# Optimization experiments

Hardware: AMD Instinct MI355X
Metric: run time of the kernel (lower is better)

## Reference

```python
import jax, jax.numpy as jnp
import numpy as np

RADIUS = 0.3      # extents/2, extents = radius_scale*6*particle_radius = 4*6*0.025 = 0.6
KSIZE = 4         # kernel_size [4,4,4]
KMAX = 80         # padded neighbor count
N = 50000
BOX = 5.2         # box side -> ~40 neighbors within RADIUS on average
CIN = 3
COUT = 3
_PI = 3.14159265358979323846


def _build_neighbors(pos, radius, kmax):
    # fixed-radius search (L2), ignore_query_point=True, padded to kmax per row
    n = pos.shape[0]
    r2 = radius * radius
    sq = (pos * pos).sum(1)
    idx = np.zeros((n, kmax), np.int32)
    msk = np.zeros((n, kmax), np.bool_)
    ch = 2500
    for s in range(0, n, ch):
        e = min(s + ch, n)
        d2 = sq[s:e, None] + sq[None, :] - 2.0 * (pos[s:e] @ pos.T)
        d2[np.arange(e - s), np.arange(s, e)] = np.inf  # radius_search_ignore_query_points
        rows, cols = np.nonzero(d2 < r2)
        starts = np.searchsorted(rows, np.arange(e - s))
        slot = np.arange(len(rows)) - starts[rows]
        keep = slot < kmax
        idx[rows[keep] + s, slot[keep]] = cols[keep]
        msk[rows[keep] + s, slot[keep]] = True
    return idx, msk


def setup_inputs():
    key = jax.random.key(0)
    k1, k2, k3 = jax.random.split(key, 3)
    pos = jax.random.uniform(k1, (N, 3), jnp.float32) * BOX
    vel = jax.random.normal(k2, (N, 3), jnp.float32)
    # keras 'uniform' initializer: U(-0.05, 0.05)
    kernel = jax.random.uniform(k3, (KSIZE, KSIZE, KSIZE, CIN, COUT), jnp.float32, -0.05, 0.05)
    nidx, nmask = _build_neighbors(np.asarray(pos), RADIUS, KMAX)
    return {"pos": pos, "vel": vel, "kernel": kernel,
            "neighbor_idx": jnp.asarray(nidx), "neighbor_mask": jnp.asarray(nmask)}


def _ball_to_cube_volume_preserving(u):
    # Open3D CoordinateTransformation.h: MapSphereToCylinder then MapCylinderToCube
    eps = 1e-12
    x, y, z = u[..., 0], u[..., 1], u[..., 2]
    sq = x * x + y * y + z * z
    norm = jnp.sqrt(jnp.maximum(sq, eps))
    sq_xy = x * x + y * y
    # sphere -> cylinder
    top = (1.25 * z * z) > sq_xy
    s_top = jnp.sqrt(3.0 * norm / (norm + jnp.abs(z)))
    s_side = norm / jnp.sqrt(jnp.maximum(sq_xy, eps))
    x1 = jnp.where(top, x * s_top, x * s_side)
    y1 = jnp.where(top, y * s_top, y * s_side)
    z1 = jnp.where(top, jnp.sign(z) * norm, 1.5 * z)
    small = sq < eps
    x1 = jnp.where(small, x, x1)
    y1 = jnp.where(small, y, y1)
    z1 = jnp.where(small, z, z1)
    # cylinder -> cube (equal-area disc->square on xy)
    sq_xy1 = x1 * x1 + y1 * y1
    norm_xy = jnp.sqrt(jnp.maximum(sq_xy1, eps))
    xbig = jnp.abs(y1) <= jnp.abs(x1)
    sx = jnp.sign(x1) * norm_xy
    sy = jnp.sign(y1) * norm_xy
    safe_x = jnp.where(jnp.abs(x1) > eps, x1, 1.0)
    safe_y = jnp.where(jnp.abs(y1) > eps, y1, 1.0)
    x2 = jnp.where(xbig, sx, sy * (4.0 / _PI) * jnp.arctan(x1 / safe_y))
    y2 = jnp.where(xbig, sx * (4.0 / _PI) * jnp.arctan(y1 / safe_x), sy)
    small_xy = sq_xy1 < eps
    x2 = jnp.where(small_xy, x1, x2)
    y2 = jnp.where(small_xy, y1, y2)
    return x2, y2, z1


def _grid_coords(c):
    # align_corners=True: [-1,1] -> [0, KSIZE-1]; 'linear' interpolation clamps to border
    t = jnp.clip((c + 1.0) * (0.5 * (KSIZE - 1)), 0.0, KSIZE - 1.0)
    t0 = jnp.floor(t)
    i0 = t0.astype(jnp.int32)
    i1 = jnp.minimum(i0 + 1, KSIZE - 1)
    f = t - t0
    return (i0, i1), (1.0 - f, f)


def _cconv(pos, vel, kernel, neighbor_idx, neighbor_mask):
    n = pos.shape[0]
    rel = pos[neighbor_idx] - pos[:, None, :]              # [N,K,3]
    d2 = jnp.sum(rel * rel, -1)
    # window_poly6 on squared distance normalized by radius^2
    imp = jnp.clip((1.0 - d2 / (RADIUS * RADIUS)) ** 3, 0.0, 1.0)
    imp = imp * neighbor_mask.astype(vel.dtype)
    cx, cy, cz = _ball_to_cube_volume_preserving(rel / RADIUS)
    (xi0, xi1), (wx0, wx1) = _grid_coords(cx)
    (yi0, yi1), (wy0, wy1) = _grid_coords(cy)
    (zi0, zi1), (wz0, wz1) = _grid_coords(cz)
    phi = vel[neighbor_idx] * imp[..., None]               # [N,K,Cin]
    rows = jnp.arange(n)[:, None]
    # accumulate window*trilinear-weighted features into the 64 filter taps,
    # then contract once with the flattened kernel (math identical to per-pair
    # interp(W) @ feat since everything is linear)
    A = jnp.zeros((n, KSIZE * KSIZE * KSIZE, vel.shape[1]), vel.dtype)
    for zi, wz in ((zi0, wz0), (zi1, wz1)):
        for yi, wy in ((yi0, wy0), (yi1, wy1)):
            for xi, wx in ((xi0, wx0), (xi1, wx1)):
                corner = (zi * KSIZE + yi) * KSIZE + xi
                A = A.at[rows, corner].add((wz * wy * wx)[..., None] * phi)
    Wflat = kernel.reshape(KSIZE * KSIZE * KSIZE, kernel.shape[3], kernel.shape[4])
    return jnp.einsum('ngi,gio->no', A, Wflat)        # [N, COUT]


def reference(pos, vel, kernel, neighbor_idx, neighbor_mask):
    return _cconv(pos, vel, kernel, neighbor_idx, neighbor_mask)
```

## Files before the change

### kernel.cpp

```cpp
#include <hip/hip_runtime.h>
#include <math.h>

#define N_PART 50000
#define KMAX 80
#define KS 4
#define LPP 16

typedef __attribute__((ext_vector_type(8))) _Float16 h8;
typedef __attribute__((ext_vector_type(2))) _Float16 h2;

__device__ __forceinline__ float atan_poly(float t) {
    float t2 = t * t;
    float p = -0.01172120f;
    p = p * t2 + 0.05265332f;
    p = p * t2 - 0.11643287f;
    p = p * t2 + 0.19354346f;
    p = p * t2 - 0.33262347f;
    p = p * t2 + 0.99997726f;
    return t * p;
}

template <typename MT>
__device__ __forceinline__ int prefix_count(const MT* __restrict__ nmask, int base, int sub) {
    int lc = 0; bool more = true;
    #pragma unroll
    for (int i = 0; i < 5; ++i) {
        bool t = nmask[base + sub * 5 + i] != 0;
        lc += (more && t) ? 1 : 0;
        more = more && t;
    }
    bool full = (lc == 5);
    unsigned long long nb = __ballot(!full);
    int wl  = threadIdx.x & 63;
    int grp = wl >> 4;
    unsigned int gb = (unsigned int)((nb >> (16 * grp)) & 0xFFFFull);
    if (gb == 0) return KMAX;
    int fi  = __ffs(gb) - 1;
    int flc = __shfl(lc, (grp << 4) + fi, 64);
    return fi * 5 + flc;
}

struct PV { float px, py, pz, ux, uy, uz; };

__device__ __forceinline__ void load_pv(const float* __restrict__ pos,
                                        const float* __restrict__ vel,
                                        int i, PV& v) {
    v.px = pos[3*i];  v.py = pos[3*i+1];  v.pz = pos[3*i+2];
    v.ux = vel[3*i];  v.uy = vel[3*i+1];  v.uz = vel[3*i+2];
}

__device__ __forceinline__ void pair_contrib(
    const PV& n, float cpx, float cpy, float cpz,
    const _Float16* __restrict__ WsH, const float* __restrict__ Ws8,
    float& acc0, float& acc1, float& acc2)
{
    const float inv_r = 1.0f / 0.3f;
    const float eps   = 1e-12f;
    const float FOUR_OVER_PI = 1.27323954473516268615f;

    float rx = (n.px - cpx) * inv_r;
    float ry = (n.py - cpy) * inv_r;
    float rz = (n.pz - cpz) * inv_r;

    float sq = rx * rx + ry * ry + rz * rz;

    float t1  = 1.0f - sq;
    float imp = fmaxf(t1 * t1 * t1, 0.0f);

    float norm   = sqrtf(fmaxf(sq, eps));
    float sq_xy  = rx * rx + ry * ry;
    bool  top    = (1.25f * rz * rz) > sq_xy;
    float rsq_xy = __builtin_amdgcn_rsqf(fmaxf(sq_xy, eps));
    float s_top  = sqrtf(3.0f * norm * __builtin_amdgcn_rcpf(norm + fabsf(rz)));
    float s_side = norm * rsq_xy;
    float s  = top ? s_top : s_side;
    float z1 = top ? copysignf(norm, rz) : 1.5f * rz;

    float nxy = top ? (sq_xy * rsq_xy * s_top) : norm;
    bool  xb  = fabsf(ry) <= fabsf(rx);
    float num = xb ? ry : rx;
    float den = xb ? rx : ry;
    float sden = (fabsf(den) > eps) ? den : 1.0f;
    float t    = num * __builtin_amdgcn_rcpf(sden);
    float at   = atan_poly(t);
    float sd   = copysignf(nxy, den);
    float u    = sd * FOUR_OVER_PI * at;
    float x2   = xb ? sd : u;
    float y2   = xb ? u  : sd;

    float tx = fminf(fmaxf((x2 + 1.0f) * 1.5f, 0.0f), 3.0f);
    float ty = fminf(fmaxf((y2 + 1.0f) * 1.5f, 0.0f), 3.0f);
    float tz = fminf(fmaxf((z1 + 1.0f) * 1.5f, 0.0f), 3.0f);
    float fx0 = floorf(tx), fy0 = floorf(ty), fz0 = floorf(tz);
    int xi0 = (int)fx0, yi0 = (int)fy0, zi0 = (int)fz0;
    int xi1 = min(xi0 + 1, KS - 1);
    int yi1 = min(yi0 + 1, KS - 1);
    int zi1 = min(zi0 + 1, KS - 1);
    float wx1 = tx - fx0, wx0 = 1.0f - wx1;
    float wy1 = ty - fy0, wy0 = 1.0f - wy1;
    float wz1 = tz - fz0, wz0 = 1.0f - wz1;

    int   zia[2] = { zi0 << 4, zi1 << 4 };  float wza[2] = { wz0, wz1 };
    int   yia[2] = { yi0 << 2, yi1 << 2 };  float wya[2] = { wy0, wy1 };
    int   xia[2] = { xi0, xi1 };            float wxa[2] = { wx0, wx1 };

    h2 M01 = (h2)(_Float16)0.0f;
    h2 M23 = (h2)(_Float16)0.0f;
    h2 M45 = (h2)(_Float16)0.0f;
    h2 M67 = (h2)(_Float16)0.0f;
    float m8 = 0.0f;

    #pragma unroll
    for (int cz = 0; cz < 2; ++cz) {
        #pragma unroll
        for (int cy = 0; cy < 2; ++cy) {
            float wzy = wza[cz] * wya[cy];
            int   czy = zia[cz] + yia[cy];
            #pragma unroll
            for (int cx = 0; cx < 2; ++cx) {
                int corner = czy + xia[cx];
                h8 wv = *(const h8*)&WsH[corner << 3];
                float wf = wzy * wxa[cx];
                _Float16 wh = (_Float16)wf;
                h2 ww = { wh, wh };
                M01 += ww * __builtin_shufflevector(wv, wv, 0, 1);
                M23 += ww * __builtin_shufflevector(wv, wv, 2, 3);
                M45 += ww * __builtin_shufflevector(wv, wv, 4, 5);
                M67 += ww * __builtin_shufflevector(wv, wv, 6, 7);
                m8  += wf * Ws8[corner];
            }
        }
    }

    float m0 = (float)M01[0], m1 = (float)M01[1];
    float m2 = (float)M23[0], m3 = (float)M23[1];
    float m4 = (float)M45[0], m5 = (float)M45[1];
    float m6 = (float)M67[0], m7 = (float)M67[1];
    float s0 = n.ux * m0 + n.uy * m3 + n.uz * m6;
    float s1 = n.ux * m1 + n.uy * m4 + n.uz * m7;
    float s2 = n.ux * m2 + n.uy * m5 + n.uz * m8;
    acc0 += imp * s0;
    acc1 += imp * s1;
    acc2 += imp * s2;
}

__global__ __launch_bounds__(256) void cconv_kernel(
    const float* __restrict__ pos,
    const float* __restrict__ vel,
    const float* __restrict__ Wg,
    const int* __restrict__ nidx,
    const void* __restrict__ nmask,
    float* __restrict__ out)
{
    __shared__ _Float16 WsH[64 * 8];
    __shared__ float    Ws8[64];
    for (int t = threadIdx.x; t < 64 * 8; t += blockDim.x) {
        int g = t >> 3, r = t & 7;
        WsH[t] = (_Float16)Wg[g * 9 + r];
    }
    for (int t = threadIdx.x; t < 64; t += blockDim.x)
        Ws8[t] = Wg[t * 9 + 8];
    __syncthreads();

    int gid = blockIdx.x * blockDim.x + threadIdx.x;
    int p   = gid >> 4;
    int sub = gid & 15;
    if (p >= N_PART) return;

    const int base = p * KMAX;

    int idxs[5];
    #pragma unroll
    for (int m = 0; m < 5; ++m)
        idxs[m] = nidx[base + sub + (m << 4)];

    bool byteMask;
    {
        const unsigned* mw = (const unsigned*)nmask;
        int lane = threadIdx.x & 63;
        bool big = false;
        #pragma unroll
        for (int i = 0; i < 8; ++i)
            big |= (mw[lane + 64 * i] > 1u);
        byteMask = (__ballot(big) != 0ULL);
    }

    float cpx = pos[3 * p], cpy = pos[3 * p + 1], cpz = pos[3 * p + 2];

    int cnt;
    if (byteMask) cnt = prefix_count<unsigned char>((const unsigned char*)nmask, base, sub);
    else          cnt = prefix_count<int>((const int*)nmask, base, sub);

    PV A, An;
    load_pv(pos, vel, idxs[0], A);

    float acc0 = 0.0f, acc1 = 0.0f, acc2 = 0.0f;

    int m = 0;
    for (int k = sub; k < cnt; k += LPP) {
        int mn = min(m + 1, 4);
        load_pv(pos, vel, idxs[mn], An);

        pair_contrib(A, cpx, cpy, cpz, WsH, Ws8, acc0, acc1, acc2);

        A = An; ++m;
    }

    acc0 += __shfl_xor(acc0, 1); acc0 += __shfl_xor(acc0, 2);
    acc0 += __shfl_xor(acc0, 4); acc0 += __shfl_xor(acc0, 8);
    acc1 += __shfl_xor(acc1, 1); acc1 += __shfl_xor(acc1, 2);
    acc1 += __shfl_xor(acc1, 4); acc1 += __shfl_xor(acc1, 8);
    acc2 += __shfl_xor(acc2, 1); acc2 += __shfl_xor(acc2, 2);
    acc2 += __shfl_xor(acc2, 4); acc2 += __shfl_xor(acc2, 8);

    if (sub == 0) {
        out[p * 3 + 0] = acc0;
        out[p * 3 + 1] = acc1;
        out[p * 3 + 2] = acc2;
    }
}

extern "C" void kernel_launch(void* const* d_in, const int* in_sizes, int n_in,
                              void* d_out, int out_size, void* d_ws, size_t ws_size,
                              hipStream_t stream) {
    const float* pos   = (const float*)d_in[0];
    const float* vel   = (const float*)d_in[1];
    const float* Wg    = (const float*)d_in[2];
    const int*   nidx  = (const int*)d_in[3];
    const void*  nmask = d_in[4];
    float*       out   = (float*)d_out;

    int threads = 256;
    long long total = (long long)N_PART * LPP;
    int grid = (int)((total + threads - 1) / threads);
    cconv_kernel<<<grid, threads, 0, stream>>>(pos, vel, Wg, nidx, nmask, out);
}
```

Measured before the change: 29.16 us.

## Pad weights to 16 halves, use fract for weights, simplify neighbor count

Packs the 9 per-tap weights into a padded 16-half shared row so the ninth channel is accumulated in packed fp16 instead of a separate fp32 load and FMA. Replaces floor/subtract with int truncation plus fractf and folds the grid offset into an FMA. Replaces the ballot/ffs prefix-count with a strided mask popcount reduced by xor shuffles, and drops the dead s_side computation. The new count assumes masks are contiguous prefixes, accumulates the ninth channel at lower precision, and removing the p>=N_PART guard relies on the grid dividing exactly.

```diff
diff --git a/kernel.cpp b/kernel.cpp
--- a/kernel.cpp
+++ b/kernel.cpp
@@ -20,26 +20,6 @@
     return t * p;
 }
 
-template <typename MT>
-__device__ __forceinline__ int prefix_count(const MT* __restrict__ nmask, int base, int sub) {
-    int lc = 0; bool more = true;
-    #pragma unroll
-    for (int i = 0; i < 5; ++i) {
-        bool t = nmask[base + sub * 5 + i] != 0;
-        lc += (more && t) ? 1 : 0;
-        more = more && t;
-    }
-    bool full = (lc == 5);
-    unsigned long long nb = __ballot(!full);
-    int wl  = threadIdx.x & 63;
-    int grp = wl >> 4;
-    unsigned int gb = (unsigned int)((nb >> (16 * grp)) & 0xFFFFull);
-    if (gb == 0) return KMAX;
-    int fi  = __ffs(gb) - 1;
-    int flc = __shfl(lc, (grp << 4) + fi, 64);
-    return fi * 5 + flc;
-}
-
 struct PV { float px, py, pz, ux, uy, uz; };
 
 __device__ __forceinline__ void load_pv(const float* __restrict__ pos,
@@ -51,7 +31,7 @@
 
 __device__ __forceinline__ void pair_contrib(
     const PV& n, float cpx, float cpy, float cpz,
-    const _Float16* __restrict__ WsH, const float* __restrict__ Ws8,
+    const _Float16* __restrict__ WsHP,
     float& acc0, float& acc1, float& acc2)
 {
     const float inv_r = 1.0f / 0.3f;
@@ -72,8 +52,6 @@
     bool  top    = (1.25f * rz * rz) > sq_xy;
     float rsq_xy = __builtin_amdgcn_rsqf(fmaxf(sq_xy, eps));
     float s_top  = sqrtf(3.0f * norm * __builtin_amdgcn_rcpf(norm + fabsf(rz)));
-    float s_side = norm * rsq_xy;
-    float s  = top ? s_top : s_side;
     float z1 = top ? copysignf(norm, rz) : 1.5f * rz;
 
     float nxy = top ? (sq_xy * rsq_xy * s_top) : norm;
@@ -88,17 +66,17 @@
     float x2   = xb ? sd : u;
     float y2   = xb ? u  : sd;
 
-    float tx = fminf(fmaxf((x2 + 1.0f) * 1.5f, 0.0f), 3.0f);
-    float ty = fminf(fmaxf((y2 + 1.0f) * 1.5f, 0.0f), 3.0f);
-    float tz = fminf(fmaxf((z1 + 1.0f) * 1.5f, 0.0f), 3.0f);
-    float fx0 = floorf(tx), fy0 = floorf(ty), fz0 = floorf(tz);
-    int xi0 = (int)fx0, yi0 = (int)fy0, zi0 = (int)fz0;
+    float tx = fminf(fmaxf(x2 * 1.5f + 1.5f, 0.0f), 3.0f);
+    float ty = fminf(fmaxf(y2 * 1.5f + 1.5f, 0.0f), 3.0f);
+    float tz = fminf(fmaxf(z1 * 1.5f + 1.5f, 0.0f), 3.0f);
+    int xi0 = (int)tx, yi0 = (int)ty, zi0 = (int)tz;
+    float wx1 = __builtin_amdgcn_fractf(tx);
+    float wy1 = __builtin_amdgcn_fractf(ty);
+    float wz1 = __builtin_amdgcn_fractf(tz);
     int xi1 = min(xi0 + 1, KS - 1);
     int yi1 = min(yi0 + 1, KS - 1);
     int zi1 = min(zi0 + 1, KS - 1);
-    float wx1 = tx - fx0, wx0 = 1.0f - wx1;
-    float wy1 = ty - fy0, wy0 = 1.0f - wy1;
-    float wz1 = tz - fz0, wz0 = 1.0f - wz1;
+    float wx0 = 1.0f - wx1, wy0 = 1.0f - wy1, wz0 = 1.0f - wz1;
 
     int   zia[2] = { zi0 << 4, zi1 << 4 };  float wza[2] = { wz0, wz1 };
     int   yia[2] = { yi0 << 2, yi1 << 2 };  float wya[2] = { wy0, wy1 };
@@ -108,7 +86,7 @@
     h2 M23 = (h2)(_Float16)0.0f;
     h2 M45 = (h2)(_Float16)0.0f;
     h2 M67 = (h2)(_Float16)0.0f;
-    float m8 = 0.0f;
+    h2 M89 = (h2)(_Float16)0.0f;
 
     #pragma unroll
     for (int cz = 0; cz < 2; ++cz) {
@@ -119,15 +97,17 @@
             #pragma unroll
             for (int cx = 0; cx < 2; ++cx) {
                 int corner = czy + xia[cx];
-                h8 wv = *(const h8*)&WsH[corner << 3];
+                const _Float16* Wc = &WsHP[corner << 4];
+                h8 lo = *(const h8*)Wc;
+                h2 hi = *(const h2*)(Wc + 8);
                 float wf = wzy * wxa[cx];
                 _Float16 wh = (_Float16)wf;
                 h2 ww = { wh, wh };
-                M01 += ww * __builtin_shufflevector(wv, wv, 0, 1);
-                M23 += ww * __builtin_shufflevector(wv, wv, 2, 3);
-                M45 += ww * __builtin_shufflevector(wv, wv, 4, 5);
-                M67 += ww * __builtin_shufflevector(wv, wv, 6, 7);
-                m8  += wf * Ws8[corner];
+                M01 += ww * __builtin_shufflevector(lo, lo, 0, 1);
+                M23 += ww * __builtin_shufflevector(lo, lo, 2, 3);
+                M45 += ww * __builtin_shufflevector(lo, lo, 4, 5);
+                M67 += ww * __builtin_shufflevector(lo, lo, 6, 7);
+                M89 += ww * hi;
             }
         }
     }
@@ -136,6 +116,7 @@
     float m2 = (float)M23[0], m3 = (float)M23[1];
     float m4 = (float)M45[0], m5 = (float)M45[1];
     float m6 = (float)M67[0], m7 = (float)M67[1];
+    float m8 = (float)M89[0];
     float s0 = n.ux * m0 + n.uy * m3 + n.uz * m6;
     float s1 = n.ux * m1 + n.uy * m4 + n.uz * m7;
     float s2 = n.ux * m2 + n.uy * m5 + n.uz * m8;
@@ -152,20 +133,16 @@
     const void* __restrict__ nmask,
     float* __restrict__ out)
 {
-    __shared__ _Float16 WsH[64 * 8];
-    __shared__ float    Ws8[64];
-    for (int t = threadIdx.x; t < 64 * 8; t += blockDim.x) {
-        int g = t >> 3, r = t & 7;
-        WsH[t] = (_Float16)Wg[g * 9 + r];
-    }
-    for (int t = threadIdx.x; t < 64; t += blockDim.x)
-        Ws8[t] = Wg[t * 9 + 8];
+    __shared__ _Float16 WsHP[64 * 16];
+    for (int t = threadIdx.x; t < 64 * 16; t += blockDim.x) {
+        int g = t >> 4, r = t & 15;
+        WsHP[t] = (r < 9) ? (_Float16)Wg[g * 9 + r] : (_Float16)0.0f;
+    }
     __syncthreads();
 
     int gid = blockIdx.x * blockDim.x + threadIdx.x;
     int p   = gid >> 4;
     int sub = gid & 15;
-    if (p >= N_PART) return;
 
     const int base = p * KMAX;
 
@@ -187,9 +164,19 @@
 
     float cpx = pos[3 * p], cpy = pos[3 * p + 1], cpz = pos[3 * p + 2];
 
-    int cnt;
-    if (byteMask) cnt = prefix_count<unsigned char>((const unsigned char*)nmask, base, sub);
-    else          cnt = prefix_count<int>((const int*)nmask, base, sub);
+    int lc = 0;
+    if (byteMask) {
+        const unsigned char* mb = (const unsigned char*)nmask;
+        #pragma unroll
+        for (int m = 0; m < 5; ++m) lc += (mb[base + sub + (m << 4)] != 0);
+    } else {
+        const int* mi = (const int*)nmask;
+        #pragma unroll
+        for (int m = 0; m < 5; ++m) lc += (mi[base + sub + (m << 4)] != 0);
+    }
+    lc += __shfl_xor(lc, 1); lc += __shfl_xor(lc, 2);
+    lc += __shfl_xor(lc, 4); lc += __shfl_xor(lc, 8);
+    const int cnt = lc;
 
     PV A, An;
     load_pv(pos, vel, idxs[0], A);
@@ -201,7 +188,7 @@
         int mn = min(m + 1, 4);
         load_pv(pos, vel, idxs[mn], An);
 
-        pair_contrib(A, cpx, cpy, cpz, WsH, Ws8, acc0, acc1, acc2);
+        pair_contrib(A, cpx, cpy, cpz, WsHP, acc0, acc1, acc2);
 
         A = An; ++m;
     }
```

New measurement: 29.52 us. Within noise of the previous version (+1.2%).
